# Optimization experiments

Measured on AMD Instinct MI355X. Metric: run time of the kernel, lower is better.

Reference implementation:

```python
import jax, jax.numpy as jnp
import numpy as np

WINDOW = 8
HEADS = 16
HIDDEN = 256
EMBED = HIDDEN * WINDOW          # 2048
HEAD_DIM = EMBED // HEADS        # 128
BATCH = 8
SEQ = 4096                       # multiple of WINDOW
GROUP = SEQ // WINDOW            # 512


def _indices():
    # index_one[i*g + j] = j*w + i  (residue-class grouping permutation)
    i = np.arange(WINDOW)
    j = np.arange(GROUP)
    index_one = (j[None, :] * WINDOW + i[:, None]).reshape(-1)
    # index_two[i*w + k] = k*g + i  (inverse-style interleave permutation)
    index_two = (np.arange(WINDOW)[None, :] * GROUP + np.arange(GROUP)[:, None]).reshape(-1)
    return jnp.asarray(index_one), jnp.asarray(index_two)


def _attention(M, Wq, Wk, Wv, fc_w, fc_b):
    # M: [N, g, E] with E = heads*head_dim
    N, L, E = M.shape
    x = M.reshape(N, L, HEADS, HEAD_DIM)
    q = jnp.einsum('nlhd,ed->nlhe', x, Wq)
    k = jnp.einsum('nlhd,ed->nlhe', x, Wk)
    v = jnp.einsum('nlhd,ed->nlhe', x, Wv)
    energy = jnp.einsum('nqhd,nkhd->nhqk', q, k)
    attn = jax.nn.softmax(energy / jnp.sqrt(jnp.float32(EMBED)), axis=-1)
    out = jnp.einsum('nhqk,nkhd->nqhd', attn, v).reshape(N, L, E)
    return out @ fc_w.T + fc_b


def setup_inputs() -> dict:
    key = jax.random.key(0)
    ks = jax.random.split(key, 6)
    s = 0.02
    return {
        'M': jax.random.normal(ks[0], (BATCH, SEQ, HIDDEN), jnp.float32),
        'Wq': jax.random.normal(ks[1], (HEAD_DIM, HEAD_DIM), jnp.float32) * s,
        'Wk': jax.random.normal(ks[2], (HEAD_DIM, HEAD_DIM), jnp.float32) * s,
        'Wv': jax.random.normal(ks[3], (HEAD_DIM, HEAD_DIM), jnp.float32) * s,
        'fc_w': jax.random.normal(ks[4], (EMBED, EMBED), jnp.float32) * s,
        'fc_b': jax.random.normal(ks[5], (EMBED,), jnp.float32) * s,
        'device': 0,
    }


def reference(M, Wq, Wk, Wv, fc_w, fc_b, device):
    del device  # unused, mirrors torch signature
    index_one, index_two = _indices()
    N, S, H = M.shape
    w, g = WINDOW, GROUP
    for b in range(w):
        idx = (index_one - b) % S
        M = M[:, idx]                                             # gather permute
        # segmentation step 1: [N, w*g, H] -> [N, g, w*H]
        M = M.reshape(N, w, g, H).transpose(0, 2, 1, 3).reshape(N, g, w * H)
        M = _attention(M, Wq, Wk, Wv, fc_w, fc_b)
        # segmentation step 2: [N, g, w*H] -> [N, w*g, H]
        M = M.reshape(N, g, w, H).transpose(0, 2, 1, 3).reshape(N, w * g, H)
        # index_two rotated once per iteration after the first -> roll by -b
        M = M[:, jnp.roll(index_two, -b)]
    return M[:, :S]
```

## Files before the change

kernel.cpp:

```cpp
#include <hip/hip_runtime.h>
#include <stdint.h>

typedef unsigned short u16;
typedef unsigned int u32;
typedef __bf16 bf16x8 __attribute__((ext_vector_type(8)));
typedef float f32x4 __attribute__((ext_vector_type(4)));
typedef float f32x16 __attribute__((ext_vector_type(16)));
typedef u16 u16x4 __attribute__((ext_vector_type(4)));
typedef u16 u16x8 __attribute__((ext_vector_type(8)));

#define MFMA16(a, b, c) __builtin_amdgcn_mfma_f32_16x16x32_bf16(a, b, c, 0, 0, 0)
#define MFMA32(a, b, c) __builtin_amdgcn_mfma_f32_32x32x16_bf16(a, b, c, 0, 0, 0)

__device__ __forceinline__ u16 f2bf(float f) {
  u32 u = __builtin_bit_cast(u32, f);
  u += 0x7FFFu + ((u >> 16) & 1u);
  return (u16)(u >> 16);
}

__device__ __forceinline__ bf16x8 ld16(const u16* p) {
  return __builtin_bit_cast(bf16x8, *(const uint4*)p);
}

__device__ __forceinline__ void gl_lds(const u16* src, u16* lds) {
  __builtin_amdgcn_global_load_lds(
      (const __attribute__((address_space(1))) u32*)src,
      (__attribute__((address_space(3))) u32*)lds, 16, 0, 0);
}

__global__ __launch_bounds__(256) void convert_weights(
    const float* __restrict__ Wq, const float* __restrict__ Wk,
    const float* __restrict__ Wv, const float* __restrict__ fcw,
    const float* __restrict__ M, u16* __restrict__ wq_b,
    u16* __restrict__ wk_b, u16* __restrict__ wv_b, u16* __restrict__ fcw_b,
    u16* __restrict__ Sb) {
  int bx = blockIdx.x, tid = threadIdx.x;
  if (bx < 4096) {
    int i = (bx * 256 + tid) * 4;
    float4 f = *(const float4*)&fcw[i];
    u16x4 o = {f2bf(f.x), f2bf(f.y), f2bf(f.z), f2bf(f.w)};
    *(u16x4*)&fcw_b[i] = o;
  } else if (bx < 4112) {
    int i = ((bx - 4096) * 256 + tid) * 4;
    const float sc = 0.022097086912079612f;
    float4 q = *(const float4*)&Wq[i];
    u16x4 oq = {f2bf(q.x * sc), f2bf(q.y * sc), f2bf(q.z * sc), f2bf(q.w * sc)};
    *(u16x4*)&wq_b[i] = oq;
    float4 k = *(const float4*)&Wk[i];
    u16x4 ok = {f2bf(k.x), f2bf(k.y), f2bf(k.z), f2bf(k.w)};
    *(u16x4*)&wk_b[i] = ok;
    float4 v = *(const float4*)&Wv[i];
    u16x4 ov = {f2bf(v.x), f2bf(v.y), f2bf(v.z), f2bf(v.w)};
    *(u16x4*)&wv_b[i] = ov;
  } else {
    size_t i = ((size_t)(bx - 4112) * 256 + tid) * 8;
    float4 f0 = *(const float4*)&M[i];
    float4 f1 = *(const float4*)&M[i + 4];
    u16x8 v = {f2bf(f0.x), f2bf(f0.y), f2bf(f0.z), f2bf(f0.w),
               f2bf(f1.x), f2bf(f1.y), f2bf(f1.z), f2bf(f1.w)};
    *(u16x8*)&Sb[i] = v;
  }
}

__global__ __launch_bounds__(512) void kv_kernel(
    const u16* __restrict__ srcB, const u16* __restrict__ wk,
    const u16* __restrict__ wvw, u16* __restrict__ K, u16* __restrict__ Vt,
    int bsh) {
  __shared__ u16 X[64 * 264];
  int jt = blockIdx.x, i0 = blockIdx.y, n = blockIdx.z;
  int tid = threadIdx.x;
#pragma unroll
  for (int it = 0; it < 4; ++it) {
    int c = tid + it * 512;
    int row = c >> 5, seg = c & 31;
    int pos = (8 * (jt * 64 + row) + i0 - bsh) & 4095;
    size_t base = ((size_t)n * 4096 + pos) * 256 + seg * 8;
    *(u16x8*)&X[row * 264 + seg * 8] = *(const u16x8*)&srcB[base];
  }
  __syncthreads();
  int wvid = tid >> 6, ln = tid & 63;
  int mat = wvid >> 2, hc = wvid & 3;
  int hh = hc >> 1, cb = (hc & 1) * 64;
  int h = i0 * 2 + hh, xc = hh * 128;
  const u16* W = (mat == 0) ? wk : wvw;
  int lr = ln & 15, lg = ln >> 4;
  f32x4 acc[4][4] = {};
#pragma unroll
  for (int kt = 0; kt < 4; ++kt) {
    bf16x8 a[4], b[4];
#pragma unroll
    for (int mt = 0; mt < 4; ++mt)
      a[mt] = ld16(&X[(mt * 16 + lr) * 264 + xc + kt * 32 + lg * 8]);
#pragma unroll
    for (int nc = 0; nc < 4; ++nc)
      b[nc] = ld16(&W[(cb + nc * 16 + lr) * 128 + kt * 32 + lg * 8]);
#pragma unroll
    for (int mt = 0; mt < 4; ++mt)
#pragma unroll
      for (int nc = 0; nc < 4; ++nc)
        acc[mt][nc] = MFMA16(a[mt], b[nc], acc[mt][nc]);
  }
  size_t nh = (size_t)(n * 16 + h);
  if (mat == 0) {
    u16* dst = K + nh * 512 * 128;
#pragma unroll
    for (int mt = 0; mt < 4; ++mt)
#pragma unroll
      for (int nc = 0; nc < 4; ++nc) {
        int col = cb + nc * 16 + lr;
        int jb = jt * 64 + mt * 16 + lg * 4;
#pragma unroll
        for (int r = 0; r < 4; ++r)
          dst[(size_t)(jb + r) * 128 + col] = f2bf(acc[mt][nc][r]);
      }
  } else {
    u16* dst = Vt + nh * 128 * 512;
#pragma unroll
    for (int mt = 0; mt < 4; ++mt)
#pragma unroll
      for (int nc = 0; nc < 4; ++nc) {
        int col = cb + nc * 16 + lr;
        int jb = jt * 64 + mt * 16 + lg * 4;
        u16x4 pk = {f2bf(acc[mt][nc][0]), f2bf(acc[mt][nc][1]),
                    f2bf(acc[mt][nc][2]), f2bf(acc[mt][nc][3])};
        *(u16x4*)&dst[(size_t)col * 512 + jb] = pk;
      }
  }
}

__global__ __launch_bounds__(512, 1) void attn_kernel(
    const u16* __restrict__ Sb, const u16* __restrict__ wq,
    const u16* __restrict__ K, const u16* __restrict__ Vt,
    u16* __restrict__ O, int bsh) {
  __shared__ u16 SMEM[40960];
#define KLp(b) (&SMEM[(b) * 8192])
#define VLp(b) (&SMEM[24576 + (b) * 8192])
#define WQB 8192
  int flat = blockIdx.x;
  int xcd = flat & 7, idx = flat >> 3;
  int gl = idx & 15, qtb = idx >> 4;
  int g = xcd | (gl << 3);
  int h = g & 15, n = g >> 4;
  int tid = threadIdx.x, wv = tid >> 6, ln = tid & 63;
  int l31 = ln & 31, hh = ln >> 5;
  size_t nh = (size_t)(n * 16 + h);
  int q0 = qtb * 256 + wv * 32;
  const u16* Kb = K + (size_t)nh * 512 * 128;
  const u16* Vb = Vt + (size_t)nh * 128 * 512;
  int i0h = h >> 1, c0 = (h & 1) * 128;

  int rK[2], cK[2], rV[2], cV[2];
#pragma unroll
  for (int i = 0; i < 2; ++i) {
    int s = wv * 2 + i;
    rK[i] = 4 * s + (ln >> 4);
    cK[i] = ((ln & 15) ^ (rK[i] & 15)) * 8;
    rV[i] = 8 * s + (ln >> 3);
    cV[i] = ((ln & 7) ^ (rV[i] & 7)) * 8;
  }

#define STAGE_K(buf, kv)                                                     \
  {                                                                          \
    const u16* kp_ = Kb + (size_t)(kv) * 64 * 128;                           \
    _Pragma("unroll") for (int i_ = 0; i_ < 2; ++i_) {                       \
      int s_ = wv * 2 + i_;                                                  \
      gl_lds(&kp_[(size_t)rK[i_] * 128 + cK[i_]], &KLp(buf)[s_ * 512]);      \
    }                                                                        \
  }
#define STAGE_V(buf, kv)                                                     \
  {                                                                          \
    _Pragma("unroll") for (int i_ = 0; i_ < 2; ++i_) {                       \
      int s_ = wv * 2 + i_;                                                  \
      gl_lds(&Vb[(size_t)rV[i_] * 512 + (kv)*64 + cV[i_]], &VLp(buf)[s_ * 512]); \
    }                                                                        \
  }

#pragma unroll
  for (int i = 0; i < 4; ++i) {
    int s = wv * 4 + i;
    int rw = 4 * s + (ln >> 4);
    int slot = (ln & 15) ^ (rw & 15);
    gl_lds(&wq[rw * 128 + slot * 8], &SMEM[WQB + s * 512]);
  }
  STAGE_K(0, 0);
  STAGE_V(1, 0);
  __syncthreads();

  int jr = wv * 32 + l31;
  int posx = (8 * (qtb * 256 + jr) + i0h - bsh) & 4095;
  const u16* xrow = Sb + ((size_t)n * 4096 + posx) * 256 + c0 + hh * 8;
  bf16x8 xf[8];
#pragma unroll
  for (int cs = 0; cs < 8; ++cs) xf[cs] = ld16(&xrow[cs * 16]);
  f32x16 qd[4] = {};
#pragma unroll
  for (int cs = 0; cs < 8; ++cs) {
#pragma unroll
    for (int eb = 0; eb < 4; ++eb) {
      int er = eb * 32 + l31;
      bf16x8 wf = ld16(&SMEM[WQB + er * 128 + ((2 * cs + hh) ^ (er & 15)) * 8]);
      qd[eb] = MFMA32(wf, xf[cs], qd[eb]);
    }
  }
  bf16x8 qf[8];
#pragma unroll
  for (int kt = 0; kt < 8; ++kt) {
    const int eb = kt >> 1, r0 = 8 * (kt & 1);
    u32 wA, wB, wC, wD;
    asm("v_cvt_pk_bf16_f32 %0, %1, %2" : "=v"(wA) : "v"(qd[eb][r0 + 0]), "v"(qd[eb][r0 + 1]));
    asm("v_cvt_pk_bf16_f32 %0, %1, %2" : "=v"(wB) : "v"(qd[eb][r0 + 2]), "v"(qd[eb][r0 + 3]));
    asm("v_cvt_pk_bf16_f32 %0, %1, %2" : "=v"(wC) : "v"(qd[eb][r0 + 4]), "v"(qd[eb][r0 + 5]));
    asm("v_cvt_pk_bf16_f32 %0, %1, %2" : "=v"(wD) : "v"(qd[eb][r0 + 6]), "v"(qd[eb][r0 + 7]));
    asm("v_permlane32_swap_b32 %0, %1" : "+v"(wA), "+v"(wC));
    asm("v_permlane32_swap_b32 %0, %1" : "+v"(wB), "+v"(wD));
    uint4 ww = {wA, wB, wC, wD};
    qf[kt] = __builtin_bit_cast(bf16x8, ww);
  }
  __syncthreads();

  STAGE_K(1, 1);

  f32x16 o[4] = {};
  float m = -1e30f, l = 0.f;

#pragma unroll
  for (int t = 0; t < 8; ++t) {
    if (t < 7) STAGE_V(t & 1, t + 1);
    if (t < 6) STAGE_K((t + 2) % 3, t + 2);
    f32x16 s[2] = {};
#pragma unroll
    for (int kt = 0; kt < 8; ++kt) {
      int slot0 = (2 * kt + hh) ^ (l31 & 15);
      bf16x8 a0 = ld16(&KLp(t % 3)[l31 * 128 + slot0 * 8]);
      s[0] = MFMA32(a0, qf[kt], s[0]);
      int row1 = 32 + l31;
      int slot1 = (2 * kt + hh) ^ (row1 & 15);
      bf16x8 a1 = ld16(&KLp(t % 3)[row1 * 128 + slot1 * 8]);
      s[1] = MFMA32(a1, qf[kt], s[1]);
    }
    float mx[8];
#pragma unroll
    for (int i = 0; i < 8; ++i)
      mx[i] = fmaxf(fmaxf(s[0][2 * i], s[0][2 * i + 1]),
                    fmaxf(s[1][2 * i], s[1][2 * i + 1]));
    float pm = fmaxf(fmaxf(fmaxf(mx[0], mx[1]), fmaxf(mx[2], mx[3])),
                     fmaxf(fmaxf(mx[4], mx[5]), fmaxf(mx[6], mx[7])));
    pm = fmaxf(pm, __shfl_xor(pm, 32));
    if (!__all(pm <= m + 8.f)) {
      float nm = fmaxf(m, pm);
      float al = __expf(m - nm);
      l *= al;
      m = nm;
#pragma unroll
      for (int r = 0; r < 16; ++r) {
        int qr = (r & 3) + 8 * (r >> 2) + 4 * hh;
        float av = __shfl(al, (ln & 32) | qr, 64);
        o[0][r] *= av; o[1][r] *= av; o[2][r] *= av; o[3][r] *= av;
      }
    }
#pragma unroll
    for (int kb2 = 0; kb2 < 2; ++kb2)
#pragma unroll
      for (int r = 0; r < 16; ++r) s[kb2][r] = __expf(s[kb2][r] - m);
    float sm[8];
#pragma unroll
    for (int i = 0; i < 8; ++i)
      sm[i] = (s[0][2 * i] + s[0][2 * i + 1]) + (s[1][2 * i] + s[1][2 * i + 1]);
    float rs = ((sm[0] + sm[1]) + (sm[2] + sm[3])) +
               ((sm[4] + sm[5]) + (sm[6] + sm[7]));
    rs += __shfl_xor(rs, 32);
    l += rs;
    bf16x8 pa[4];
#pragma unroll
    for (int ks = 0; ks < 4; ++ks) {
      const int kb2 = ks >> 1, r0 = 8 * (ks & 1);
      u32 wA, wB, wC, wD;
      asm("v_cvt_pk_bf16_f32 %0, %1, %2" : "=v"(wA) : "v"(s[kb2][r0 + 0]), "v"(s[kb2][r0 + 1]));
      asm("v_cvt_pk_bf16_f32 %0, %1, %2" : "=v"(wB) : "v"(s[kb2][r0 + 2]), "v"(s[kb2][r0 + 3]));
      asm("v_cvt_pk_bf16_f32 %0, %1, %2" : "=v"(wC) : "v"(s[kb2][r0 + 4]), "v"(s[kb2][r0 + 5]));
      asm("v_cvt_pk_bf16_f32 %0, %1, %2" : "=v"(wD) : "v"(s[kb2][r0 + 6]), "v"(s[kb2][r0 + 7]));
      asm("v_permlane32_swap_b32 %0, %1" : "+v"(wA), "+v"(wC));
      asm("v_permlane32_swap_b32 %0, %1" : "+v"(wB), "+v"(wD));
      uint4 ww = {wA, wB, wC, wD};
      pa[ks] = __builtin_bit_cast(bf16x8, ww);
    }
    __builtin_amdgcn_s_setprio(1);
#pragma unroll
    for (int ks = 0; ks < 4; ++ks)
#pragma unroll
      for (int nb = 0; nb < 4; ++nb) {
        int row = nb * 32 + l31;
        int slot = (2 * ks + hh) ^ (row & 7);
        bf16x8 bv = ld16(&VLp((t + 1) & 1)[row * 64 + slot * 8]);
        o[nb] = MFMA32(pa[ks], bv, o[nb]);
      }
    __builtin_amdgcn_s_setprio(0);
    if (t < 6) {
      asm volatile("s_waitcnt vmcnt(2)" ::: "memory");
      __builtin_amdgcn_s_barrier();
    } else if (t == 6) {
      asm volatile("s_waitcnt vmcnt(0)" ::: "memory");
      __builtin_amdgcn_s_barrier();
    }
  }
#undef STAGE_K
#undef STAGE_V
#undef KLp
#undef VLp
#undef WQB

  float inv = 1.f / l;
#pragma unroll
  for (int r = 0; r < 16; ++r) {
    int qr = (r & 3) + 8 * (r >> 2) + 4 * hh;
    float iv = __shfl(inv, (ln & 32) | qr, 64);
    int row = q0 + qr;
    u16* dst = O + ((size_t)n * 512 + row) * 2048 + h * 128;
    dst[0 * 32 + l31] = f2bf(o[0][r] * iv);
    dst[1 * 32 + l31] = f2bf(o[1][r] * iv);
    dst[2 * 32 + l31] = f2bf(o[2][r] * iv);
    dst[3 * 32 + l31] = f2bf(o[3][r] * iv);
  }
}

__global__ __launch_bounds__(512, 1) void fc_kernel(
    const u16* __restrict__ A, const u16* __restrict__ Bw,
    const float* __restrict__ bias, float* __restrict__ doutF,
    u16* __restrict__ doutB, int last, int bsh) {
  __shared__ u16 AL[3][256 * 64];
  __shared__ u16 BL[3][128 * 64];
  int blk = blockIdx.x;
  int xcd = blk & 7, j = blk >> 3;
  int bn = xcd * 2 + (j & 1), bm = j >> 1;
  int tid = threadIdx.x, wv = tid >> 6, ln = tid & 63;
  int lr = ln & 15, lg = ln >> 4;
  int R0 = bm * 256, C0 = bn * 128;
  int wr = (wv >> 1) * 64, wc = (wv & 1) * 64;
  const u16* gA[4];
  int sA[4];
  const u16* gB[2];
  int sB[2];
#pragma unroll
  for (int i = 0; i < 4; ++i) {
    int r = wv * 32 + i * 8 + (ln >> 3);
    int cs = ((ln & 7) ^ (r & 7)) * 8;
    gA[i] = A + (size_t)(R0 + r) * 2048 + cs;
    sA[i] = (wv * 32 + i * 8) * 64;
  }
#pragma unroll
  for (int i = 0; i < 2; ++i) {
    int r = wv * 16 + i * 8 + (ln >> 3);
    int cs = ((ln & 7) ^ (r & 7)) * 8;
    gB[i] = Bw + (size_t)(C0 + r) * 2048 + cs;
    sB[i] = (wv * 16 + i * 8) * 64;
  }
  int aoff[4][2], boff[4][2];
#pragma unroll
  for (int i = 0; i < 4; ++i) {
    int ra = wr + i * 16 + lr, rb = wc + i * 16 + lr;
#pragma unroll
    for (int kk = 0; kk < 2; ++kk) {
      aoff[i][kk] = ra * 64 + (((kk * 4 + lg) ^ (ra & 7)) * 8);
      boff[i][kk] = rb * 64 + (((kk * 4 + lg) ^ (rb & 7)) * 8);
    }
  }
  f32x4 acc[4][4] = {};

#define STAGE6(buf, k0)                          \
  {                                              \
    gl_lds(gA[0] + (k0), &AL[buf][sA[0]]);       \
    gl_lds(gA[1] + (k0), &AL[buf][sA[1]]);       \
    gl_lds(gA[2] + (k0), &AL[buf][sA[2]]);       \
    gl_lds(gA[3] + (k0), &AL[buf][sA[3]]);       \
    gl_lds(gB[0] + (k0), &BL[buf][sB[0]]);       \
    gl_lds(gB[1] + (k0), &BL[buf][sB[1]]);       \
  }

  STAGE6(0, 0);
  STAGE6(1, 64);
  asm volatile("s_waitcnt vmcnt(6)" ::: "memory");
  __builtin_amdgcn_s_barrier();

  for (int t = 0; t < 32; ++t) {
    int cur = t % 3, nx2 = (t + 2) % 3;
    int k2 = (t + 2) * 64;
    bf16x8 a0 = ld16(&AL[cur][aoff[0][0]]), a1 = ld16(&AL[cur][aoff[1][0]]);
    bf16x8 a2 = ld16(&AL[cur][aoff[2][0]]), a3 = ld16(&AL[cur][aoff[3][0]]);
    bf16x8 b0 = ld16(&BL[cur][boff[0][0]]), b1 = ld16(&BL[cur][boff[1][0]]);
    bf16x8 b2 = ld16(&BL[cur][boff[2][0]]), b3 = ld16(&BL[cur][boff[3][0]]);
    if (t < 30) {
      gl_lds(gA[0] + k2, &AL[nx2][sA[0]]);
      gl_lds(gA[1] + k2, &AL[nx2][sA[1]]);
      gl_lds(gB[0] + k2, &BL[nx2][sB[0]]);
    }
    __builtin_amdgcn_s_barrier();
    asm volatile("s_waitcnt lgkmcnt(0)" ::: "memory");
    __builtin_amdgcn_sched_barrier(0);
    __builtin_amdgcn_s_setprio(1);
    acc[0][0] = MFMA16(a0, b0, acc[0][0]);
    acc[0][1] = MFMA16(a0, b1, acc[0][1]);
    acc[0][2] = MFMA16(a0, b2, acc[0][2]);
    acc[0][3] = MFMA16(a0, b3, acc[0][3]);
    acc[1][0] = MFMA16(a1, b0, acc[1][0]);
    acc[1][1] = MFMA16(a1, b1, acc[1][1]);
    acc[1][2] = MFMA16(a1, b2, acc[1][2]);
    acc[1][3] = MFMA16(a1, b3, acc[1][3]);
    acc[2][0] = MFMA16(a2, b0, acc[2][0]);
    acc[2][1] = MFMA16(a2, b1, acc[2][1]);
    acc[2][2] = MFMA16(a2, b2, acc[2][2]);
    acc[2][3] = MFMA16(a2, b3, acc[2][3]);
    acc[3][0] = MFMA16(a3, b0, acc[3][0]);
    acc[3][1] = MFMA16(a3, b1, acc[3][1]);
    acc[3][2] = MFMA16(a3, b2, acc[3][2]);
    acc[3][3] = MFMA16(a3, b3, acc[3][3]);
    __builtin_amdgcn_s_setprio(0);
    __builtin_amdgcn_s_barrier();
    a0 = ld16(&AL[cur][aoff[0][1]]); a1 = ld16(&AL[cur][aoff[1][1]]);
    a2 = ld16(&AL[cur][aoff[2][1]]); a3 = ld16(&AL[cur][aoff[3][1]]);
    b0 = ld16(&BL[cur][boff[0][1]]); b1 = ld16(&BL[cur][boff[1][1]]);
    b2 = ld16(&BL[cur][boff[2][1]]); b3 = ld16(&BL[cur][boff[3][1]]);
    if (t < 30) {
      gl_lds(gA[2] + k2, &AL[nx2][sA[2]]);
      gl_lds(gA[3] + k2, &AL[nx2][sA[3]]);
      gl_lds(gB[1] + k2, &BL[nx2][sB[1]]);
      asm volatile("s_waitcnt vmcnt(6)" ::: "memory");
    } else if (t == 30) {
      asm volatile("s_waitcnt vmcnt(0)" ::: "memory");
    }
    __builtin_amdgcn_s_barrier();
    asm volatile("s_waitcnt lgkmcnt(0)" ::: "memory");
    __builtin_amdgcn_sched_barrier(0);
    __builtin_amdgcn_s_setprio(1);
    acc[0][0] = MFMA16(a0, b0, acc[0][0]);
    acc[0][1] = MFMA16(a0, b1, acc[0][1]);
    acc[0][2] = MFMA16(a0, b2, acc[0][2]);
    acc[0][3] = MFMA16(a0, b3, acc[0][3]);
    acc[1][0] = MFMA16(a1, b0, acc[1][0]);
    acc[1][1] = MFMA16(a1, b1, acc[1][1]);
    acc[1][2] = MFMA16(a1, b2, acc[1][2]);
    acc[1][3] = MFMA16(a1, b3, acc[1][3]);
    acc[2][0] = MFMA16(a2, b0, acc[2][0]);
    acc[2][1] = MFMA16(a2, b1, acc[2][1]);
    acc[2][2] = MFMA16(a2, b2, acc[2][2]);
    acc[2][3] = MFMA16(a2, b3, acc[2][3]);
    acc[3][0] = MFMA16(a3, b0, acc[3][0]);
    acc[3][1] = MFMA16(a3, b1, acc[3][1]);
    acc[3][2] = MFMA16(a3, b2, acc[3][2]);
    acc[3][3] = MFMA16(a3, b3, acc[3][3]);
    __builtin_amdgcn_s_setprio(0);
    __builtin_amdgcn_s_barrier();
  }
#undef STAGE6
#pragma unroll
  for (int nc = 0; nc < 4; ++nc) {
    int e = C0 + wc + nc * 16 + lr;
    float bv = bias[e];
    int i = e >> 8, cc = e & 255;
#pragma unroll
    for (int mt = 0; mt < 4; ++mt)
#pragma unroll
      for (int r = 0; r < 4; ++r) {
        int row = R0 + wr + mt * 16 + lg * 4 + r;
        int nn = row >> 9, jj = row & 511;
        int pos = (8 * jj + i - bsh) & 4095;
        size_t di = ((size_t)nn * 4096 + pos) * 256 + cc;
        float v = acc[mt][nc][r] + bv;
        if (last) doutF[di] = v;
        else doutB[di] = f2bf(v);
      }
  }
}

extern "C" void kernel_launch(void* const* d_in, const int* in_sizes, int n_in,
                              void* d_out, int out_size, void* d_ws, size_t ws_size,
                              hipStream_t stream) {
  const float* M = (const float*)d_in[0];
  const float* Wq = (const float*)d_in[1];
  const float* Wk = (const float*)d_in[2];
  const float* Wv = (const float*)d_in[3];
  const float* fcw = (const float*)d_in[4];
  const float* fcb = (const float*)d_in[5];
  float* out = (float*)d_out;
  char* ws = (char*)d_ws;
  u16* wq_b = (u16*)(ws + (0 << 10));
  u16* wk_b = (u16*)(ws + (32 << 10));
  u16* wv_b = (u16*)(ws + (64 << 10));
  u16* fcw_b = (u16*)(ws + (128 << 10));
  u16* Kb = (u16*)(ws + ((size_t)32 << 20));
  u16* Vtb = (u16*)(ws + ((size_t)48 << 20));
  u16* Ab = (u16*)(ws + ((size_t)64 << 20));
  u16* Sb = (u16*)(ws + ((size_t)96 << 20));

  convert_weights<<<8208, 256, 0, stream>>>(Wq, Wk, Wv, fcw, M, wq_b, wk_b,
                                            wv_b, fcw_b, Sb);
  for (int b = 0; b < 8; ++b) {
    kv_kernel<<<dim3(8, 8, 8), 512, 0, stream>>>(Sb, wk_b, wv_b, Kb, Vtb, b);
    attn_kernel<<<256, 512, 0, stream>>>(Sb, wq_b, Kb, Vtb, Ab, b);
    fc_kernel<<<256, 512, 0, stream>>>(Ab, fcw_b, fcb, out, Sb,
                                       (b == 7) ? 1 : 0, b);
  }
}
```

Measured before the change: 665.0 us.

## Fuse K/V projection into attention kernel, computing per-tile K and V in LDS

```diff
diff --git a/kernel.cpp b/kernel.cpp
--- a/kernel.cpp
+++ b/kernel.cpp
@@ -62,80 +62,12 @@
   }
 }
 
-__global__ __launch_bounds__(512) void kv_kernel(
-    const u16* __restrict__ srcB, const u16* __restrict__ wk,
-    const u16* __restrict__ wvw, u16* __restrict__ K, u16* __restrict__ Vt,
-    int bsh) {
-  __shared__ u16 X[64 * 264];
-  int jt = blockIdx.x, i0 = blockIdx.y, n = blockIdx.z;
-  int tid = threadIdx.x;
-#pragma unroll
-  for (int it = 0; it < 4; ++it) {
-    int c = tid + it * 512;
-    int row = c >> 5, seg = c & 31;
-    int pos = (8 * (jt * 64 + row) + i0 - bsh) & 4095;
-    size_t base = ((size_t)n * 4096 + pos) * 256 + seg * 8;
-    *(u16x8*)&X[row * 264 + seg * 8] = *(const u16x8*)&srcB[base];
-  }
-  __syncthreads();
-  int wvid = tid >> 6, ln = tid & 63;
-  int mat = wvid >> 2, hc = wvid & 3;
-  int hh = hc >> 1, cb = (hc & 1) * 64;
-  int h = i0 * 2 + hh, xc = hh * 128;
-  const u16* W = (mat == 0) ? wk : wvw;
-  int lr = ln & 15, lg = ln >> 4;
-  f32x4 acc[4][4] = {};
-#pragma unroll
-  for (int kt = 0; kt < 4; ++kt) {
-    bf16x8 a[4], b[4];
-#pragma unroll
-    for (int mt = 0; mt < 4; ++mt)
-      a[mt] = ld16(&X[(mt * 16 + lr) * 264 + xc + kt * 32 + lg * 8]);
-#pragma unroll
-    for (int nc = 0; nc < 4; ++nc)
-      b[nc] = ld16(&W[(cb + nc * 16 + lr) * 128 + kt * 32 + lg * 8]);
-#pragma unroll
-    for (int mt = 0; mt < 4; ++mt)
-#pragma unroll
-      for (int nc = 0; nc < 4; ++nc)
-        acc[mt][nc] = MFMA16(a[mt], b[nc], acc[mt][nc]);
-  }
-  size_t nh = (size_t)(n * 16 + h);
-  if (mat == 0) {
-    u16* dst = K + nh * 512 * 128;
-#pragma unroll
-    for (int mt = 0; mt < 4; ++mt)
-#pragma unroll
-      for (int nc = 0; nc < 4; ++nc) {
-        int col = cb + nc * 16 + lr;
-        int jb = jt * 64 + mt * 16 + lg * 4;
-#pragma unroll
-        for (int r = 0; r < 4; ++r)
-          dst[(size_t)(jb + r) * 128 + col] = f2bf(acc[mt][nc][r]);
-      }
-  } else {
-    u16* dst = Vt + nh * 128 * 512;
-#pragma unroll
-    for (int mt = 0; mt < 4; ++mt)
-#pragma unroll
-      for (int nc = 0; nc < 4; ++nc) {
-        int col = cb + nc * 16 + lr;
-        int jb = jt * 64 + mt * 16 + lg * 4;
-        u16x4 pk = {f2bf(acc[mt][nc][0]), f2bf(acc[mt][nc][1]),
-                    f2bf(acc[mt][nc][2]), f2bf(acc[mt][nc][3])};
-        *(u16x4*)&dst[(size_t)col * 512 + jb] = pk;
-      }
-  }
-}
-
 __global__ __launch_bounds__(512, 1) void attn_kernel(
     const u16* __restrict__ Sb, const u16* __restrict__ wq,
-    const u16* __restrict__ K, const u16* __restrict__ Vt,
+    const u16* __restrict__ wk, const u16* __restrict__ wvw,
     u16* __restrict__ O, int bsh) {
-  __shared__ u16 SMEM[40960];
-#define KLp(b) (&SMEM[(b) * 8192])
-#define VLp(b) (&SMEM[24576 + (b) * 8192])
-#define WQB 8192
+  __shared__ u16 SMEM[73728];
+  const int WKB = 0, WVB = 16384, XTB = 32768, KTB = 40960, VTB = 57344;
   int flat = blockIdx.x;
   int xcd = flat & 7, idx = flat >> 3;
   int gl = idx & 15, qtb = idx >> 4;
@@ -143,52 +75,38 @@
   int h = g & 15, n = g >> 4;
   int tid = threadIdx.x, wv = tid >> 6, ln = tid & 63;
   int l31 = ln & 31, hh = ln >> 5;
-  size_t nh = (size_t)(n * 16 + h);
   int q0 = qtb * 256 + wv * 32;
-  const u16* Kb = K + (size_t)nh * 512 * 128;
-  const u16* Vb = Vt + (size_t)nh * 128 * 512;
   int i0h = h >> 1, c0 = (h & 1) * 128;
-
-  int rK[2], cK[2], rV[2], cV[2];
-#pragma unroll
-  for (int i = 0; i < 2; ++i) {
-    int s = wv * 2 + i;
-    rK[i] = 4 * s + (ln >> 4);
-    cK[i] = ((ln & 15) ^ (rK[i] & 15)) * 8;
-    rV[i] = 8 * s + (ln >> 3);
-    cV[i] = ((ln & 7) ^ (rV[i] & 7)) * 8;
-  }
-
-#define STAGE_K(buf, kv)                                                     \
-  {                                                                          \
-    const u16* kp_ = Kb + (size_t)(kv) * 64 * 128;                           \
-    _Pragma("unroll") for (int i_ = 0; i_ < 2; ++i_) {                       \
-      int s_ = wv * 2 + i_;                                                  \
-      gl_lds(&kp_[(size_t)rK[i_] * 128 + cK[i_]], &KLp(buf)[s_ * 512]);      \
-    }                                                                        \
-  }
-#define STAGE_V(buf, kv)                                                     \
+  const u16* Xbase = Sb + (size_t)n * 4096 * 256 + c0;
+
+  int l16 = ln & 15, lrow4 = ln >> 4;
+
+#define STAGE_X(kvt)                                                         \
   {                                                                          \
     _Pragma("unroll") for (int i_ = 0; i_ < 2; ++i_) {                       \
       int s_ = wv * 2 + i_;                                                  \
-      gl_lds(&Vb[(size_t)rV[i_] * 512 + (kv)*64 + cV[i_]], &VLp(buf)[s_ * 512]); \
+      int row_ = 4 * s_ + lrow4;                                             \
+      int pos_ = (8 * ((kvt)*64 + row_) + i0h - bsh) & 4095;                 \
+      gl_lds(&Xbase[(size_t)pos_ * 256 + ((l16 ^ (row_ & 15)) * 8)],         \
+             &SMEM[XTB + s_ * 512]);                                         \
     }                                                                        \
   }
 
 #pragma unroll
   for (int i = 0; i < 4; ++i) {
     int s = wv * 4 + i;
-    int rw = 4 * s + (ln >> 4);
-    int slot = (ln & 15) ^ (rw & 15);
-    gl_lds(&wq[rw * 128 + slot * 8], &SMEM[WQB + s * 512]);
-  }
-  STAGE_K(0, 0);
-  STAGE_V(1, 0);
+    int rw = 4 * s + lrow4;
+    int slot = (l16 ^ (rw & 15)) * 8;
+    gl_lds(&wq[rw * 128 + slot], &SMEM[KTB + s * 512]);
+    gl_lds(&wk[rw * 128 + slot], &SMEM[WKB + s * 512]);
+    gl_lds(&wvw[rw * 128 + slot], &SMEM[WVB + s * 512]);
+  }
+  STAGE_X(0);
   __syncthreads();
 
   int jr = wv * 32 + l31;
   int posx = (8 * (qtb * 256 + jr) + i0h - bsh) & 4095;
-  const u16* xrow = Sb + ((size_t)n * 4096 + posx) * 256 + c0 + hh * 8;
+  const u16* xrow = Xbase + (size_t)posx * 256 + hh * 8;
   bf16x8 xf[8];
 #pragma unroll
   for (int cs = 0; cs < 8; ++cs) xf[cs] = ld16(&xrow[cs * 16]);
@@ -198,7 +116,7 @@
 #pragma unroll
     for (int eb = 0; eb < 4; ++eb) {
       int er = eb * 32 + l31;
-      bf16x8 wf = ld16(&SMEM[WQB + er * 128 + ((2 * cs + hh) ^ (er & 15)) * 8]);
+      bf16x8 wf = ld16(&SMEM[KTB + er * 128 + ((2 * cs + hh) ^ (er & 15)) * 8]);
       qd[eb] = MFMA32(wf, xf[cs], qd[eb]);
     }
   }
@@ -216,26 +134,64 @@
     uint4 ww = {wA, wB, wC, wD};
     qf[kt] = __builtin_bit_cast(bf16x8, ww);
   }
+
+  const int keblk = wv >> 1, tokblk = wv & 1;
+  bf16x8 wkf[8], wvf[8];
+  {
+    int er = keblk * 32 + l31;
+#pragma unroll
+    for (int cs = 0; cs < 8; ++cs) {
+      wkf[cs] = ld16(&SMEM[WKB + er * 128 + ((2 * cs + hh) ^ (er & 15)) * 8]);
+      wvf[cs] = ld16(&SMEM[WVB + er * 128 + ((2 * cs + hh) ^ (er & 15)) * 8]);
+    }
+  }
   __syncthreads();
 
-  STAGE_K(1, 1);
+#define PROJ(dst)                                                            \
+  {                                                                          \
+    bf16x8 xp[8];                                                            \
+    int xtok_ = tokblk * 32 + l31;                                           \
+    _Pragma("unroll") for (int cs = 0; cs < 8; ++cs)                         \
+        xp[cs] = ld16(&SMEM[XTB + xtok_ * 128 +                              \
+                            ((2 * cs + hh) ^ (xtok_ & 15)) * 8]);            \
+    f32x16 kacc = {}, vacc = {};                                             \
+    _Pragma("unroll") for (int cs = 0; cs < 8; ++cs) {                       \
+      kacc = MFMA32(xp[cs], wkf[cs], kacc);                                  \
+      vacc = MFMA32(wvf[cs], xp[cs], vacc);                                  \
+    }                                                                        \
+    int ke_ = keblk * 32 + l31;                                              \
+    _Pragma("unroll") for (int r = 0; r < 16; ++r) {                         \
+      int tok_ = tokblk * 32 + (r & 3) + 8 * (r >> 2) + 4 * hh;              \
+      SMEM[KTB + (dst)*8192 + tok_ * 128 + (((ke_ >> 3) ^ (tok_ & 15)) * 8) +\
+           (ke_ & 7)] = f2bf(kacc[r]);                                       \
+    }                                                                        \
+    _Pragma("unroll") for (int r = 0; r < 16; ++r) {                         \
+      int ev_ = keblk * 32 + (r & 3) + 8 * (r >> 2) + 4 * hh;                \
+      SMEM[VTB + (dst)*8192 + ev_ * 64 + (((xtok_ >> 3) ^ (ev_ & 7)) * 8) +  \
+           (xtok_ & 7)] = f2bf(vacc[r]);                                     \
+    }                                                                        \
+  }
+
+  PROJ(0);
+  __syncthreads();
+  STAGE_X(1);
 
   f32x16 o[4] = {};
   float m = -1e30f, l = 0.f;
 
 #pragma unroll
   for (int t = 0; t < 8; ++t) {
-    if (t < 7) STAGE_V(t & 1, t + 1);
-    if (t < 6) STAGE_K((t + 2) % 3, t + 2);
+    const int cur = t & 1;
+    const int uKT = KTB + cur * 8192, uVT = VTB + cur * 8192;
     f32x16 s[2] = {};
 #pragma unroll
     for (int kt = 0; kt < 8; ++kt) {
       int slot0 = (2 * kt + hh) ^ (l31 & 15);
-      bf16x8 a0 = ld16(&KLp(t % 3)[l31 * 128 + slot0 * 8]);
+      bf16x8 a0 = ld16(&SMEM[uKT + l31 * 128 + slot0 * 8]);
       s[0] = MFMA32(a0, qf[kt], s[0]);
       int row1 = 32 + l31;
       int slot1 = (2 * kt + hh) ^ (row1 & 15);
-      bf16x8 a1 = ld16(&KLp(t % 3)[row1 * 128 + slot1 * 8]);
+      bf16x8 a1 = ld16(&SMEM[uKT + row1 * 128 + slot1 * 8]);
       s[1] = MFMA32(a1, qf[kt], s[1]);
     }
     float mx[8];
@@ -291,23 +247,20 @@
       for (int nb = 0; nb < 4; ++nb) {
         int row = nb * 32 + l31;
         int slot = (2 * ks + hh) ^ (row & 7);
-        bf16x8 bv = ld16(&VLp((t + 1) & 1)[row * 64 + slot * 8]);
+        bf16x8 bv = ld16(&SMEM[uVT + row * 64 + slot * 8]);
         o[nb] = MFMA32(pa[ks], bv, o[nb]);
       }
     __builtin_amdgcn_s_setprio(0);
-    if (t < 6) {
-      asm volatile("s_waitcnt vmcnt(2)" ::: "memory");
-      __builtin_amdgcn_s_barrier();
-    } else if (t == 6) {
+    if (t < 7) {
       asm volatile("s_waitcnt vmcnt(0)" ::: "memory");
       __builtin_amdgcn_s_barrier();
-    }
-  }
-#undef STAGE_K
-#undef STAGE_V
-#undef KLp
-#undef VLp
-#undef WQB
+      PROJ((t + 1) & 1);
+      __builtin_amdgcn_s_barrier();
+      if (t < 6) STAGE_X(t + 2);
+    }
+  }
+#undef PROJ
+#undef STAGE_X
 
   float inv = 1.f / l;
 #pragma unroll
@@ -486,16 +439,13 @@
   u16* wk_b = (u16*)(ws + (32 << 10));
   u16* wv_b = (u16*)(ws + (64 << 10));
   u16* fcw_b = (u16*)(ws + (128 << 10));
-  u16* Kb = (u16*)(ws + ((size_t)32 << 20));
-  u16* Vtb = (u16*)(ws + ((size_t)48 << 20));
   u16* Ab = (u16*)(ws + ((size_t)64 << 20));
   u16* Sb = (u16*)(ws + ((size_t)96 << 20));
 
   convert_weights<<<8208, 256, 0, stream>>>(Wq, Wk, Wv, fcw, M, wq_b, wk_b,
                                             wv_b, fcw_b, Sb);
   for (int b = 0; b < 8; ++b) {
-    kv_kernel<<<dim3(8, 8, 8), 512, 0, stream>>>(Sb, wk_b, wv_b, Kb, Vtb, b);
-    attn_kernel<<<256, 512, 0, stream>>>(Sb, wq_b, Kb, Vtb, Ab, b);
+    attn_kernel<<<256, 512, 0, stream>>>(Sb, wq_b, wk_b, wv_b, Ab, b);
     fc_kernel<<<256, 512, 0, stream>>>(Ab, fcw_b, fcb, out, Sb,
                                        (b == 7) ? 1 : 0, b);
   }
```

After: 1.244 ms. 1.87x slower.
